# Performance work log

Hardware: AMD Instinct MI355X
Metric: run time of the kernel (lower is better)

Reference implementation:

```python
import jax, jax.numpy as jnp
import numpy as np

D = 8  # polynomial degree; with bias present, basis has D columns (P1..PD)


def setup_inputs() -> dict:
    key = jax.random.key(0)
    k1, k2 = jax.random.split(key)
    batch, n_in, n_out = 65536, 256, 64
    x = jax.random.normal(k1, (batch, n_in), dtype=jnp.float32)
    c_basis = jax.random.normal(k2, (n_out, n_in, D), dtype=jnp.float32) * (1.0 / np.sqrt(n_in * D))
    bias = jnp.zeros((n_out,), dtype=jnp.float32)
    return {"x": x, "c_basis": c_basis, "bias": bias}


def _legendre_basis(x):
    # x: (batch, n_in). Returns (batch, n_in, D) = [P1(t), ..., PD(t)], t = tanh(x).
    t = jnp.tanh(x)
    p_prev = jnp.ones_like(t)  # P0
    p_curr = t                 # P1
    polys = [p_curr]
    for k in range(2, D + 1):  # small fixed-length loop over degree
        p_next = ((2 * k - 1) * t * p_curr - (k - 1) * p_prev) / k
        polys.append(p_next)
        p_prev, p_curr = p_curr, p_next
    return jnp.stack(polys, axis=-1)  # (batch, n_in, D)


def reference(x, c_basis, bias):
    # basis: (batch, n_in, D); contract over (n_in, D) with c_basis (n_out, n_in, D)
    leg = _legendre_basis(x)
    y = jnp.einsum('bid,oid->bo', leg, c_basis)
    return y + bias
```

## Files before the change

### kernel.cpp

```cpp
#include <hip/hip_runtime.h>
#include <hip/hip_bf16.h>

typedef _Float16 half2v __attribute__((ext_vector_type(2)));
typedef _Float16 half8 __attribute__((ext_vector_type(8)));
typedef __attribute__((ext_vector_type(4))) float floatx4;
typedef __attribute__((ext_vector_type(4))) unsigned int uintx4;

#define GLOBAL_AS __attribute__((address_space(1)))
#define LDS_AS __attribute__((address_space(3)))

__device__ __forceinline__ void async_ld16(const void* g, void* l) {
  __builtin_amdgcn_global_load_lds((const GLOBAL_AS unsigned int*)g,
                                   (LDS_AS unsigned int*)l, 16, 0, 0);
}

__device__ __forceinline__ half2v h2(float v) {
  return (half2v){(_Float16)v, (_Float16)v};
}

__device__ __forceinline__ void legendre2_f16(float xv0, float xv1,
                                              half8* fa0, half8* fa1) {
  float e0 = __builtin_amdgcn_exp2f(xv0 * 2.885390081777927f);
  float t0 = 1.0f - 2.0f * __builtin_amdgcn_rcpf(e0 + 1.0f);
  float e1 = __builtin_amdgcn_exp2f(xv1 * 2.885390081777927f);
  float t1 = 1.0f - 2.0f * __builtin_amdgcn_rcpf(e1 + 1.0f);
  half2v t;
  { auto tt = __builtin_amdgcn_cvt_pkrtz(t0, t1); __builtin_memcpy(&t, &tt, 4); }
  half2v p1 = t;
  half2v u2 = t * p1, w2 = u2 - h2(1.0f);  half2v p2 = h2(0.5f)      * w2 + u2;
  half2v u3 = t * p2, w3 = u3 - p1;        half2v p3 = h2(2.0f/3.0f) * w3 + u3;
  half2v u4 = t * p3, w4 = u4 - p2;        half2v p4 = h2(0.75f)     * w4 + u4;
  half2v u5 = t * p4, w5 = u5 - p3;        half2v p5 = h2(0.8f)      * w5 + u5;
  half2v u6 = t * p5, w6 = u6 - p4;        half2v p6 = h2(5.0f/6.0f) * w6 + u6;
  half2v u7 = t * p6, w7 = u7 - p5;        half2v p7 = h2(6.0f/7.0f) * w7 + u7;
  half2v u8 = t * p7, w8 = u8 - p6;        half2v p8 = h2(7.0f/8.0f) * w8 + u8;
  unsigned P[8];
  __builtin_memcpy(&P[0], &p1, 4); __builtin_memcpy(&P[1], &p2, 4);
  __builtin_memcpy(&P[2], &p3, 4); __builtin_memcpy(&P[3], &p4, 4);
  __builtin_memcpy(&P[4], &p5, 4); __builtin_memcpy(&P[5], &p6, 4);
  __builtin_memcpy(&P[6], &p7, 4); __builtin_memcpy(&P[7], &p8, 4);
  union { unsigned u[4]; half8 h; } a0, a1;
#pragma unroll
  for (int j = 0; j < 4; ++j) {
    a0.u[j] = __builtin_amdgcn_perm(P[2*j+1], P[2*j], 0x05040100u);
    a1.u[j] = __builtin_amdgcn_perm(P[2*j+1], P[2*j], 0x07060302u);
  }
  *fa0 = a0.h;
  *fa1 = a1.h;
}

__global__ void conv_kernel(const float* __restrict__ cb, _Float16* __restrict__ ws) {
  int t = blockIdx.x * 128 + threadIdx.x;
  int o = t >> 8;
  int i = t & 255;
  const floatx4* s = (const floatx4*)(cb + ((size_t)o * 256 + i) * 8);
  floatx4 v0 = s[0], v1 = s[1];
  union { _Float16 h[8]; uintx4 u; } w;
  w.h[0] = (_Float16)v0.x; w.h[1] = (_Float16)v0.y;
  w.h[2] = (_Float16)v0.z; w.h[3] = (_Float16)v0.w;
  w.h[4] = (_Float16)v1.x; w.h[5] = (_Float16)v1.y;
  w.h[6] = (_Float16)v1.z; w.h[7] = (_Float16)v1.w;
  *(uintx4*)(ws + (size_t)i * 512 + o * 8) = w.u;
}

__global__ __launch_bounds__(128, 4) void kan_kernel(
    const float* __restrict__ x, const _Float16* __restrict__ ws,
    const float* __restrict__ bias, float* __restrict__ y) {
  __shared__ __align__(16) _Float16 bt[2][2][2048];

  const int tid  = threadIdx.x;
  const int wid  = tid >> 6;
  const int lane = tid & 63;
  const int m    = lane & 15;
  const int q    = lane >> 4;
  const int rb   = blockIdx.x * 32;

  floatx4 acc[2][4];
#pragma unroll
  for (int a = 0; a < 2; ++a)
#pragma unroll
    for (int nt = 0; nt < 4; ++nt) acc[a][nt] = (floatx4){0.f, 0.f, 0.f, 0.f};

  const _Float16* bs0 = ws + (size_t)(wid * 128 +  0) * 512 + lane * 8;
  const _Float16* bs1 = ws + (size_t)(wid * 128 + 32) * 512 + lane * 8;
  const _Float16* bs2 = ws + (size_t)(wid * 128 + 64) * 512 + lane * 8;
  const _Float16* bs3 = ws + (size_t)(wid * 128 + 96) * 512 + lane * 8;

  const float* xp0 = x + (size_t)(rb + m) * 256 + wid * 128 + q * 32;
  const float* xp1 = xp0 + 16 * 256;

  floatx4 xs0[3], xs1[3];
  xs0[0] = *(const floatx4*)(xp0);     xs1[0] = *(const floatx4*)(xp1);
  xs0[1] = *(const floatx4*)(xp0 + 4); xs1[1] = *(const floatx4*)(xp1 + 4);
  __builtin_amdgcn_sched_barrier(0);

  {
    _Float16* ld = &bt[wid][0][0];
    async_ld16(bs0, ld);        async_ld16(bs1, ld + 512);
    async_ld16(bs2, ld + 1024); async_ld16(bs3, ld + 1536);
    bs0 += 512; bs1 += 512; bs2 += 512; bs3 += 512;
  }
  __builtin_amdgcn_sched_barrier(0);

#define CHUNK(ch, N, DOX)                                                      \
  {                                                                            \
    if constexpr (DOX) {                                                       \
      constexpr int gp = (ch) / 4 + 2;                                         \
      xs0[gp % 3] = *(const floatx4*)(xp0 + gp * 4);                           \
      xs1[gp % 3] = *(const floatx4*)(xp1 + gp * 4);                           \
    }                                                                          \
    __builtin_amdgcn_sched_barrier(0);                                         \
    if constexpr ((ch) < 31) {                                                 \
      _Float16* ld = &bt[wid][((ch) + 1) & 1][0];                              \
      async_ld16(bs0, ld);        async_ld16(bs1, ld + 512);                   \
      async_ld16(bs2, ld + 1024); async_ld16(bs3, ld + 1536);                  \
      bs0 += 512; bs1 += 512; bs2 += 512; bs3 += 512;                          \
    }                                                                          \
    __builtin_amdgcn_sched_barrier(0);                                         \
    half8 f0, f1;                                                              \
    legendre2_f16(xs0[((ch) / 4) % 3][(ch) % 4],                               \
                  xs1[((ch) / 4) % 3][(ch) % 4], &f0, &f1);                    \
    asm volatile("s_waitcnt vmcnt(" #N ")" ::: "memory");                      \
    const _Float16* bp = &bt[wid][(ch) & 1][q * 512 + m * 8];                  \
    half8 fb0 = *(const half8*)(bp + 0);                                       \
    half8 fb1 = *(const half8*)(bp + 128);                                     \
    half8 fb2 = *(const half8*)(bp + 256);                                     \
    half8 fb3 = *(const half8*)(bp + 384);                                     \
    __builtin_amdgcn_s_setprio(1);                                             \
    acc[0][0] = __builtin_amdgcn_mfma_f32_16x16x32_f16(f0, fb0, acc[0][0], 0, 0, 0); \
    acc[1][0] = __builtin_amdgcn_mfma_f32_16x16x32_f16(f1, fb0, acc[1][0], 0, 0, 0); \
    acc[0][1] = __builtin_amdgcn_mfma_f32_16x16x32_f16(f0, fb1, acc[0][1], 0, 0, 0); \
    acc[1][1] = __builtin_amdgcn_mfma_f32_16x16x32_f16(f1, fb1, acc[1][1], 0, 0, 0); \
    acc[0][2] = __builtin_amdgcn_mfma_f32_16x16x32_f16(f0, fb2, acc[0][2], 0, 0, 0); \
    acc[1][2] = __builtin_amdgcn_mfma_f32_16x16x32_f16(f1, fb2, acc[1][2], 0, 0, 0); \
    acc[0][3] = __builtin_amdgcn_mfma_f32_16x16x32_f16(f0, fb3, acc[0][3], 0, 0, 0); \
    acc[1][3] = __builtin_amdgcn_mfma_f32_16x16x32_f16(f1, fb3, acc[1][3], 0, 0, 0); \
    __builtin_amdgcn_s_setprio(0);                                             \
  }

  CHUNK(0, 6, 1)  CHUNK(1, 4, 0)  CHUNK(2, 4, 0)  CHUNK(3, 4, 0)
  CHUNK(4, 6, 1)  CHUNK(5, 4, 0)  CHUNK(6, 4, 0)  CHUNK(7, 4, 0)
  CHUNK(8, 6, 1)  CHUNK(9, 4, 0)  CHUNK(10, 4, 0) CHUNK(11, 4, 0)
  CHUNK(12, 6, 1) CHUNK(13, 4, 0) CHUNK(14, 4, 0) CHUNK(15, 4, 0)
  CHUNK(16, 6, 1) CHUNK(17, 4, 0) CHUNK(18, 4, 0) CHUNK(19, 4, 0)
  CHUNK(20, 6, 1) CHUNK(21, 4, 0) CHUNK(22, 4, 0) CHUNK(23, 4, 0)
  CHUNK(24, 4, 0) CHUNK(25, 4, 0) CHUNK(26, 4, 0) CHUNK(27, 4, 0)
  CHUNK(28, 4, 0) CHUNK(29, 4, 0) CHUNK(30, 4, 0) CHUNK(31, 0, 0)
#undef CHUNK

  float* red = (float*)&bt[0][0][0];
  __syncthreads();
  if (wid) {
#pragma unroll
    for (int a = 0; a < 2; ++a)
#pragma unroll
      for (int nt = 0; nt < 4; ++nt)
        *(floatx4*)(red + ((a * 4 + nt) * 64 + lane) * 4) = acc[a][nt];
  }
  __syncthreads();
  if (!wid) {
    float bv[4];
#pragma unroll
    for (int nt = 0; nt < 4; ++nt) bv[nt] = bias[nt * 16 + m];
#pragma unroll
    for (int a = 0; a < 2; ++a) {
      int gr0 = rb + a * 16 + q * 4;
#pragma unroll
      for (int nt = 0; nt < 4; ++nt) {
        floatx4 p = *(const floatx4*)(red + ((a * 4 + nt) * 64 + lane) * 4);
#pragma unroll
        for (int r = 0; r < 4; ++r) {
          y[(size_t)(gr0 + r) * 64 + nt * 16 + m] = acc[a][nt][r] + p[r] + bv[nt];
        }
      }
    }
  }
}

extern "C" void kernel_launch(void* const* d_in, const int* in_sizes, int n_in,
                              void* d_out, int out_size, void* d_ws, size_t ws_size,
                              hipStream_t stream) {
  const float* x    = (const float*)d_in[0];
  const float* cb   = (const float*)d_in[1];
  const float* bias = (const float*)d_in[2];
  float* y = (float*)d_out;
  _Float16* ws = (_Float16*)d_ws;
  int batch = in_sizes[0] / 256;
  hipLaunchKernelGGL(conv_kernel, dim3(128), dim3(128), 0, stream, cb, ws);
  hipLaunchKernelGGL(kan_kernel, dim3(batch / 32), dim3(128), 0, stream, x, ws, bias, y);
}
```

Before: 136.0 us.

## Load B fragments directly to registers and use 4-wave blocks with nontemporal I/O

Drops the LDS double-buffer staging of the converted fp16 weights, so each lane now loads its B fragments straight from global memory (L2-resident) into registers one chunk ahead. Blocks grow to 4 waves covering 64 rows, split as 2 row-halves by 2 K-halves, with an LDS reduction across the K-halves. x loads and y stores become nontemporal to keep streaming data out of the cache. This removes LDS traffic and the explicit waitcnt bookkeeping, but every wave now re-reads the weights from global or L2, which raises cache bandwidth demand and register pressure.

```diff
diff --git a/kernel.cpp b/kernel.cpp
--- a/kernel.cpp
+++ b/kernel.cpp
@@ -5,14 +5,6 @@
 typedef _Float16 half8 __attribute__((ext_vector_type(8)));
 typedef __attribute__((ext_vector_type(4))) float floatx4;
 typedef __attribute__((ext_vector_type(4))) unsigned int uintx4;
-
-#define GLOBAL_AS __attribute__((address_space(1)))
-#define LDS_AS __attribute__((address_space(3)))
-
-__device__ __forceinline__ void async_ld16(const void* g, void* l) {
-  __builtin_amdgcn_global_load_lds((const GLOBAL_AS unsigned int*)g,
-                                   (LDS_AS unsigned int*)l, 16, 0, 0);
-}
 
 __device__ __forceinline__ half2v h2(float v) {
   return (half2v){(_Float16)v, (_Float16)v};
@@ -63,17 +55,19 @@
   *(uintx4*)(ws + (size_t)i * 512 + o * 8) = w.u;
 }
 
-__global__ __launch_bounds__(128, 4) void kan_kernel(
+__global__ __launch_bounds__(256, 4) void kan_kernel(
     const float* __restrict__ x, const _Float16* __restrict__ ws,
     const float* __restrict__ bias, float* __restrict__ y) {
-  __shared__ __align__(16) _Float16 bt[2][2][2048];
+  __shared__ __align__(16) float red[4096];
 
   const int tid  = threadIdx.x;
   const int wid  = tid >> 6;
+  const int kh   = wid >> 1;
+  const int rh   = wid & 1;
   const int lane = tid & 63;
   const int m    = lane & 15;
   const int q    = lane >> 4;
-  const int rb   = blockIdx.x * 32;
+  const int rb   = blockIdx.x * 64;
 
   floatx4 acc[2][4];
 #pragma unroll
@@ -81,96 +75,87 @@
 #pragma unroll
     for (int nt = 0; nt < 4; ++nt) acc[a][nt] = (floatx4){0.f, 0.f, 0.f, 0.f};
 
-  const _Float16* bs0 = ws + (size_t)(wid * 128 +  0) * 512 + lane * 8;
-  const _Float16* bs1 = ws + (size_t)(wid * 128 + 32) * 512 + lane * 8;
-  const _Float16* bs2 = ws + (size_t)(wid * 128 + 64) * 512 + lane * 8;
-  const _Float16* bs3 = ws + (size_t)(wid * 128 + 96) * 512 + lane * 8;
+  const _Float16* bp = ws + (size_t)(kh * 128 + q * 32) * 512 + m * 8;
 
-  const float* xp0 = x + (size_t)(rb + m) * 256 + wid * 128 + q * 32;
+  const float* xp0 = x + (size_t)(rb + rh * 32 + m) * 256 + kh * 128 + q * 32;
   const float* xp1 = xp0 + 16 * 256;
 
   floatx4 xs0[3], xs1[3];
-  xs0[0] = *(const floatx4*)(xp0);     xs1[0] = *(const floatx4*)(xp1);
-  xs0[1] = *(const floatx4*)(xp0 + 4); xs1[1] = *(const floatx4*)(xp1 + 4);
-  __builtin_amdgcn_sched_barrier(0);
+  xs0[0] = __builtin_nontemporal_load((const floatx4*)(xp0));
+  xs1[0] = __builtin_nontemporal_load((const floatx4*)(xp1));
+  xs0[1] = __builtin_nontemporal_load((const floatx4*)(xp0 + 4));
+  xs1[1] = __builtin_nontemporal_load((const floatx4*)(xp1 + 4));
 
-  {
-    _Float16* ld = &bt[wid][0][0];
-    async_ld16(bs0, ld);        async_ld16(bs1, ld + 512);
-    async_ld16(bs2, ld + 1024); async_ld16(bs3, ld + 1536);
-    bs0 += 512; bs1 += 512; bs2 += 512; bs3 += 512;
-  }
-  __builtin_amdgcn_sched_barrier(0);
+  half8 bc0 = *(const half8*)(bp + 0);
+  half8 bc1 = *(const half8*)(bp + 128);
+  half8 bc2 = *(const half8*)(bp + 256);
+  half8 bc3 = *(const half8*)(bp + 384);
+  bp += 512;
 
-#define CHUNK(ch, N, DOX)                                                      \
+#define CHUNK(ch, DOX)                                                         \
   {                                                                            \
+    half8 bn0, bn1, bn2, bn3;                                                  \
+    if constexpr ((ch) < 31) {                                                 \
+      bn0 = *(const half8*)(bp + 0);                                           \
+      bn1 = *(const half8*)(bp + 128);                                         \
+      bn2 = *(const half8*)(bp + 256);                                         \
+      bn3 = *(const half8*)(bp + 384);                                         \
+      bp += 512;                                                               \
+    }                                                                          \
     if constexpr (DOX) {                                                       \
       constexpr int gp = (ch) / 4 + 2;                                         \
-      xs0[gp % 3] = *(const floatx4*)(xp0 + gp * 4);                           \
-      xs1[gp % 3] = *(const floatx4*)(xp1 + gp * 4);                           \
+      xs0[gp % 3] = __builtin_nontemporal_load((const floatx4*)(xp0 + gp * 4));\
+      xs1[gp % 3] = __builtin_nontemporal_load((const floatx4*)(xp1 + gp * 4));\
     }                                                                          \
-    __builtin_amdgcn_sched_barrier(0);                                         \
-    if constexpr ((ch) < 31) {                                                 \
-      _Float16* ld = &bt[wid][((ch) + 1) & 1][0];                              \
-      async_ld16(bs0, ld);        async_ld16(bs1, ld + 512);                   \
-      async_ld16(bs2, ld + 1024); async_ld16(bs3, ld + 1536);                  \
-      bs0 += 512; bs1 += 512; bs2 += 512; bs3 += 512;                          \
-    }                                                                          \
-    __builtin_amdgcn_sched_barrier(0);                                         \
     half8 f0, f1;                                                              \
     legendre2_f16(xs0[((ch) / 4) % 3][(ch) % 4],                               \
                   xs1[((ch) / 4) % 3][(ch) % 4], &f0, &f1);                    \
-    asm volatile("s_waitcnt vmcnt(" #N ")" ::: "memory");                      \
-    const _Float16* bp = &bt[wid][(ch) & 1][q * 512 + m * 8];                  \
-    half8 fb0 = *(const half8*)(bp + 0);                                       \
-    half8 fb1 = *(const half8*)(bp + 128);                                     \
-    half8 fb2 = *(const half8*)(bp + 256);                                     \
-    half8 fb3 = *(const half8*)(bp + 384);                                     \
     __builtin_amdgcn_s_setprio(1);                                             \
-    acc[0][0] = __builtin_amdgcn_mfma_f32_16x16x32_f16(f0, fb0, acc[0][0], 0, 0, 0); \
-    acc[1][0] = __builtin_amdgcn_mfma_f32_16x16x32_f16(f1, fb0, acc[1][0], 0, 0, 0); \
-    acc[0][1] = __builtin_amdgcn_mfma_f32_16x16x32_f16(f0, fb1, acc[0][1], 0, 0, 0); \
-    acc[1][1] = __builtin_amdgcn_mfma_f32_16x16x32_f16(f1, fb1, acc[1][1], 0, 0, 0); \
-    acc[0][2] = __builtin_amdgcn_mfma_f32_16x16x32_f16(f0, fb2, acc[0][2], 0, 0, 0); \
-    acc[1][2] = __builtin_amdgcn_mfma_f32_16x16x32_f16(f1, fb2, acc[1][2], 0, 0, 0); \
-    acc[0][3] = __builtin_amdgcn_mfma_f32_16x16x32_f16(f0, fb3, acc[0][3], 0, 0, 0); \
-    acc[1][3] = __builtin_amdgcn_mfma_f32_16x16x32_f16(f1, fb3, acc[1][3], 0, 0, 0); \
+    acc[0][0] = __builtin_amdgcn_mfma_f32_16x16x32_f16(f0, bc0, acc[0][0], 0, 0, 0); \
+    acc[1][0] = __builtin_amdgcn_mfma_f32_16x16x32_f16(f1, bc0, acc[1][0], 0, 0, 0); \
+    acc[0][1] = __builtin_amdgcn_mfma_f32_16x16x32_f16(f0, bc1, acc[0][1], 0, 0, 0); \
+    acc[1][1] = __builtin_amdgcn_mfma_f32_16x16x32_f16(f1, bc1, acc[1][1], 0, 0, 0); \
+    acc[0][2] = __builtin_amdgcn_mfma_f32_16x16x32_f16(f0, bc2, acc[0][2], 0, 0, 0); \
+    acc[1][2] = __builtin_amdgcn_mfma_f32_16x16x32_f16(f1, bc2, acc[1][2], 0, 0, 0); \
+    acc[0][3] = __builtin_amdgcn_mfma_f32_16x16x32_f16(f0, bc3, acc[0][3], 0, 0, 0); \
+    acc[1][3] = __builtin_amdgcn_mfma_f32_16x16x32_f16(f1, bc3, acc[1][3], 0, 0, 0); \
     __builtin_amdgcn_s_setprio(0);                                             \
+    if constexpr ((ch) < 31) { bc0 = bn0; bc1 = bn1; bc2 = bn2; bc3 = bn3; }   \
   }
 
-  CHUNK(0, 6, 1)  CHUNK(1, 4, 0)  CHUNK(2, 4, 0)  CHUNK(3, 4, 0)
-  CHUNK(4, 6, 1)  CHUNK(5, 4, 0)  CHUNK(6, 4, 0)  CHUNK(7, 4, 0)
-  CHUNK(8, 6, 1)  CHUNK(9, 4, 0)  CHUNK(10, 4, 0) CHUNK(11, 4, 0)
-  CHUNK(12, 6, 1) CHUNK(13, 4, 0) CHUNK(14, 4, 0) CHUNK(15, 4, 0)
-  CHUNK(16, 6, 1) CHUNK(17, 4, 0) CHUNK(18, 4, 0) CHUNK(19, 4, 0)
-  CHUNK(20, 6, 1) CHUNK(21, 4, 0) CHUNK(22, 4, 0) CHUNK(23, 4, 0)
-  CHUNK(24, 4, 0) CHUNK(25, 4, 0) CHUNK(26, 4, 0) CHUNK(27, 4, 0)
-  CHUNK(28, 4, 0) CHUNK(29, 4, 0) CHUNK(30, 4, 0) CHUNK(31, 0, 0)
+  CHUNK(0, 1)  CHUNK(1, 0)  CHUNK(2, 0)  CHUNK(3, 0)
+  CHUNK(4, 1)  CHUNK(5, 0)  CHUNK(6, 0)  CHUNK(7, 0)
+  CHUNK(8, 1)  CHUNK(9, 0)  CHUNK(10, 0) CHUNK(11, 0)
+  CHUNK(12, 1) CHUNK(13, 0) CHUNK(14, 0) CHUNK(15, 0)
+  CHUNK(16, 1) CHUNK(17, 0) CHUNK(18, 0) CHUNK(19, 0)
+  CHUNK(20, 1) CHUNK(21, 0) CHUNK(22, 0) CHUNK(23, 0)
+  CHUNK(24, 0) CHUNK(25, 0) CHUNK(26, 0) CHUNK(27, 0)
+  CHUNK(28, 0) CHUNK(29, 0) CHUNK(30, 0) CHUNK(31, 0)
 #undef CHUNK
 
-  float* red = (float*)&bt[0][0][0];
   __syncthreads();
-  if (wid) {
+  if (kh) {
 #pragma unroll
     for (int a = 0; a < 2; ++a)
 #pragma unroll
       for (int nt = 0; nt < 4; ++nt)
-        *(floatx4*)(red + ((a * 4 + nt) * 64 + lane) * 4) = acc[a][nt];
+        *(floatx4*)(red + ((rh * 8 + a * 4 + nt) * 64 + lane) * 4) = acc[a][nt];
   }
   __syncthreads();
-  if (!wid) {
+  if (!kh) {
     float bv[4];
 #pragma unroll
     for (int nt = 0; nt < 4; ++nt) bv[nt] = bias[nt * 16 + m];
 #pragma unroll
     for (int a = 0; a < 2; ++a) {
-      int gr0 = rb + a * 16 + q * 4;
+      int gr0 = rb + rh * 32 + a * 16 + q * 4;
 #pragma unroll
       for (int nt = 0; nt < 4; ++nt) {
-        floatx4 p = *(const floatx4*)(red + ((a * 4 + nt) * 64 + lane) * 4);
+        floatx4 p = *(const floatx4*)(red + ((rh * 8 + a * 4 + nt) * 64 + lane) * 4);
 #pragma unroll
         for (int r = 0; r < 4; ++r) {
-          y[(size_t)(gr0 + r) * 64 + nt * 16 + m] = acc[a][nt][r] + p[r] + bv[nt];
+          float v = acc[a][nt][r] + p[r] + bv[nt];
+          __builtin_nontemporal_store(v, &y[(size_t)(gr0 + r) * 64 + nt * 16 + m]);
         }
       }
     }
@@ -187,5 +172,5 @@
   _Float16* ws = (_Float16*)d_ws;
   int batch = in_sizes[0] / 256;
   hipLaunchKernelGGL(conv_kernel, dim3(128), dim3(128), 0, stream, cb, ws);
-  hipLaunchKernelGGL(kan_kernel, dim3(batch / 32), dim3(128), 0, stream, x, ws, bias, y);
+  hipLaunchKernelGGL(kan_kernel, dim3(batch / 64), dim3(256), 0, stream, x, ws, bias, y);
 }
```

Result: slower. 151.1 us (+11.1%).
